# Kernel optimization log

Hardware: AMD Instinct MI355X
Metric: run time of the kernel (lower is better)

Reference implementation:

```python
import jax, jax.numpy as jnp
import numpy as np

SIGMA = 0.1   # sigma_disc (params[3])
ALPHA = 0.05  # alpha_disc (params[2])


def setup_inputs() -> dict:
    key = jax.random.key(0)
    k1, k2, k3 = jax.random.split(key, 3)
    E, S, T = 3, 8192, 100  # num_events, num_samples, num_bin + num_extra_bin
    logits = jax.random.normal(k1, (E, S, T), dtype=jnp.float32)
    event_out = jax.nn.softmax(logits, axis=-1)  # per-event discrete hazard probs, rows sum to 1
    event_times = jax.random.randint(k2, (S, E), 0, 99).astype(jnp.int32)
    labs = jax.random.randint(k3, (S, E), 0, 2).astype(jnp.int32)
    return {"event_out": event_out, "event_times": event_times, "labs": labs,
            "num_bin": 96, "num_extra_bin": 4}


def _c_loss(event_out, event_times, labs, T):
    # cum[e, k, t] = sum(event_out[e, k, :t+1]); risk with cutoff c = 1 - cum[..., c-1]
    cum = jnp.cumsum(event_out, axis=-1)  # (E, S, T)
    E = event_out.shape[0]
    penalty = jnp.float32(0.0)
    for i in range(E):  # small fixed number of events
        c = cum[i]                    # (S, T)
        t = event_times[:, i]         # (S,)
        lab = labs[:, i]              # (S,)
        had = lab == 1
        # ---- forward concordance (had_event branch) ----
        e_f = jnp.minimum(t + 1, T - 1)              # per-reference-sample cutoff, >= 1
        # risk_f[j, k] = 1 - sum(event_out[k, :e_f[j]]) = 1 - cum[k, e_f[j]-1]
        risk_f = 1.0 - c[:, e_f - 1].T               # (S_j, S_k)
        diff_f = risk_f - jnp.diagonal(risk_f)[:, None]  # comp_risk - reference_risk
        # f_compare: t_k > e_j - 1  OR  (t_k == e_j - 1 AND lab_k == 0)
        mask_f = had[:, None] & ((t[None, :] >= e_f[:, None]) |
                                 ((t[None, :] == e_f[:, None] - 1) & (lab[None, :] == 0)))
        penalty = penalty + jnp.sum(jnp.where(mask_f & (diff_f < 0),
                                              jnp.exp(-diff_f / SIGMA), 0.0))
        # ---- backward concordance (back_c branch, active when t_j > 0) ----
        e_b = jnp.minimum(jnp.where(had, t, t + 1), T - 1)
        risk_b = 1.0 - c[:, jnp.maximum(e_b, 1) - 1].T
        diff_b = risk_b - jnp.diagonal(risk_b)[:, None]
        # b_compare: t_k <= e_j - 1 AND lab_k == 1
        mask_b = (t > 0)[:, None] & (t[None, :] <= e_b[:, None] - 1) & (lab[None, :] == 1)
        penalty = penalty + jnp.sum(jnp.where(mask_b & (diff_b > 0),
                                              jnp.exp(diff_b / SIGMA), 0.0))
    return ALPHA * penalty


def reference(event_out, event_times, labs, num_bin, num_extra_bin):
    return _c_loss(event_out, event_times, labs, num_bin + num_extra_bin)
```

## Files before the change

### kernel.cpp

```cpp
#include <hip/hip_runtime.h>

#define E_CONST 3
#define T_CONST 100
#define C10 10.0f
#define ALPHA_C 0.05f
#define SPLIT 4
#define MAXK 8192
#define NGROUP (E_CONST * 2 * T_CONST)

__device__ inline int waveInclScan(int v, int lane) {
    #pragma unroll
    for (int off = 1; off < 64; off <<= 1) {
        int n = __shfl_up(v, off, 64);
        if (lane >= off) v += n;
    }
    return v;
}

__global__ __launch_bounds__(512) void prep_kernel(
    const float* __restrict__ event_out, float* __restrict__ cumT, int S)
{
    __shared__ float tile[64][101];
    const int tid = threadIdx.x;
    const int rowbase = (int)blockIdx.x * 64;
    const float4* __restrict__ src =
        reinterpret_cast<const float4*>(event_out) + (size_t)rowbase * 25;
    for (int idx = tid; idx < 64 * 25; idx += 512) {
        const float4 v = src[idx];
        const int r = idx / 25;
        const int c = idx - r * 25;
        float* d = &tile[r][c * 4];
        d[0] = v.x; d[1] = v.y; d[2] = v.z; d[3] = v.w;
    }
    __syncthreads();
    if (tid < 64) {
        float run = 0.f;
        #pragma unroll 4
        for (int c = 0; c < T_CONST; ++c) { run += tile[tid][c]; tile[tid][c] = run; }
    }
    __syncthreads();
    const int i  = rowbase / S;
    const int s0 = rowbase - i * S;
    float* __restrict__ dst = cumT + (size_t)i * T_CONST * S + s0;
    for (int idx = tid; idx < 64 * T_CONST; idx += 512) {
        const int t = idx >> 6;
        const int r = idx & 63;
        dst[(size_t)t * S + r] = tile[r][t];
    }
}

__global__ __launch_bounds__(256) void thrfill_kernel(
    const float* __restrict__ cumT, const int* __restrict__ et,
    const int* __restrict__ labs, float* __restrict__ thrVals,
    int* __restrict__ gCnt, int S)
{
    __shared__ int wcnt[4];
    const int tid = threadIdx.x;
    const int lane = tid & 63, wid = tid >> 6;
    const int gid = (int)blockIdx.x;
    const int i = gid / 200;
    const int r = gid - i * 200;
    const int dir = r / 100;
    const int tt = r - dir * 100;

    const int colIdx = tt;
    int t1 = 0, t2 = -1;
    bool any = true;
    if (dir == 0) { t1 = tt; }
    else {
        const int cb = tt;
        if (cb >= T_CONST - 1) any = false;
        t1 = cb + 1;
        if (cb > 0) t2 = cb;
    }

    int cnt = 0;
    if (any) {
        const float* __restrict__ col = cumT + ((size_t)i * T_CONST + colIdx) * S;
        float* __restrict__ dst = thrVals + (size_t)gid * MAXK;
        for (int s0 = 0; s0 < S; s0 += 1024) {
            const int sb = s0 + tid * 4;
            const float4 cv = *reinterpret_cast<const float4*>(col + sb);
            float tv[4]; int mask = 0, m = 0;
            #pragma unroll
            for (int j = 0; j < 4; ++j) {
                const int s = sb + j;
                const int ts = et[s * E_CONST + i];
                const int ls = labs[s * E_CONST + i];
                const float c = (j == 0) ? cv.x : (j == 1) ? cv.y
                              : (j == 2) ? cv.z : cv.w;
                tv[j] = __expf(C10 * c);
                const bool p = ((ts == t1) & (ls == 1)) |
                               ((t2 >= 0) & (ts == t2) & (ls == 0));
                if (p) { mask |= (1 << j); ++m; }
            }
            const int incl = waveInclScan(m, lane);
            if (lane == 63) wcnt[wid] = incl;
            __syncthreads();
            int base = cnt + incl - m;
            for (int w = 0; w < wid; ++w) base += wcnt[w];
            #pragma unroll
            for (int j = 0; j < 4; ++j)
                if (mask & (1 << j)) dst[base++] = tv[j];
            cnt += wcnt[0] + wcnt[1] + wcnt[2] + wcnt[3];
            __syncthreads();
        }
    }
    if (tid == 0) gCnt[gid] = cnt;
}

__global__ __launch_bounds__(256) void grouppair_kernel(
    const float* __restrict__ cumT, const float* __restrict__ thrVals,
    const int* __restrict__ gCnt, const int* __restrict__ et,
    const int* __restrict__ labs, float* __restrict__ partials, int S)
{
    __shared__ __align__(16) float elds[2048];
    __shared__ float wsum[4];
    __shared__ int wcnt[4];
    __shared__ int nTot;
    const int tid = threadIdx.x;
    const int lane = tid & 63, wid = tid >> 6;

    int x = (int)blockIdx.x;
    const int sp = x & (SPLIT - 1); x >>= 2;
    const int dir = x & 1;          x >>= 1;
    const int tt = x % T_CONST;
    const int i  = x / T_CONST;

    int colIdx = 0, tref = 0, tgid = 0;
    bool active = true;
    if (dir == 0) { colIdx = tt; tref = tt; tgid = i * 200 + tt; }
    else {
        const int cb = (T_CONST - 2) - tt;
        if (cb < 0) active = false;
        else { colIdx = cb; tref = cb; tgid = i * 200 + 100 + cb; }
    }
    const int K = active ? gCnt[tgid] : 0;
    if (K <= 0) active = false;

    float blocktot = 0.f;
    if (active) {
        const float* __restrict__ col = cumT + ((size_t)i * T_CONST + colIdx) * S;
        const float sgn = (dir == 0) ? C10 : -C10;
        const int chunk = S / SPLIT;
        const int cbeg = sp * chunk;

        float ev[8];
        int mask = 0, m = 0;
        #pragma unroll
        for (int j = 0; j < 8; ++j) {
            const int s = cbeg + tid + j * 256;
            const int ts = et[s * E_CONST + i];
            const int ls = labs[s * E_CONST + i];
            const bool mem = (dir == 0)
                ? ((ts > tref) | ((ts == tref) & (ls == 0)))
                : ((ts <= tref) & (ls == 1));
            ev[j] = __expf(sgn * col[s]);
            if (mem) { mask |= (1 << j); ++m; }
        }
        const int incl = waveInclScan(m, lane);
        if (lane == 63) wcnt[wid] = incl;
        __syncthreads();
        int off = 0;
        for (int w = 0; w < wid; ++w) off += wcnt[w];
        int base = incl - m + off;
        #pragma unroll
        for (int j = 0; j < 8; ++j)
            if (mask & (1 << j)) elds[base++] = ev[j];
        if (tid == 255) {
            nTot = base;
            const int np = (base + 3) & ~3;
            for (int p = base; p < np; ++p) elds[p] = 0.f;
        }
        __syncthreads();

        const int n = nTot;
        if (n > 0) {
            const int qn4 = ((n + 3) & ~3) >> 2;
            const int kq = tid & 31;
            const int ep = tid >> 5;
            const float4* __restrict__ e4 = reinterpret_cast<const float4*>(elds);
            const float* __restrict__ tv = thrVals + (size_t)tgid * MAXK;
            const int nkc = (K + 31) >> 5;

            for (int kc = 0; kc < nkc; ++kc) {
                const int j = (kc << 5) + kq;
                float thr = 1e30f, factor = 0.f;
                if (j < K) {
                    const float tval = tv[j];
                    if (dir == 0) { thr = tval;        factor = 1.0f / tval; }
                    else          { thr = 1.0f / tval; factor = tval; }
                }
                float acc = 0.f;
                for (int q = ep; q < qn4; q += 8) {
                    const float4 v = e4[q];
                    acc += (v.x > thr) ? v.x : 0.f;
                    acc += (v.y > thr) ? v.y : 0.f;
                    acc += (v.z > thr) ? v.z : 0.f;
                    acc += (v.w > thr) ? v.w : 0.f;
                }
                blocktot += acc * factor;
            }
        }
    }

    for (int off = 32; off > 0; off >>= 1) blocktot += __shfl_down(blocktot, off, 64);
    if (lane == 0) wsum[wid] = blocktot;
    __syncthreads();
    if (tid == 0) partials[blockIdx.x] = wsum[0] + wsum[1] + wsum[2] + wsum[3];
}

__global__ __launch_bounds__(1024) void reduce_kernel(
    const float* __restrict__ partials, int n, float* __restrict__ out)
{
    const int tid = threadIdx.x;
    float s0 = 0.f, s1 = 0.f, s2 = 0.f, s3 = 0.f;
    const int n4 = n & ~3;
    for (int idx = tid * 4; idx < n4; idx += 4096) {
        const float4 v = *reinterpret_cast<const float4*>(partials + idx);
        s0 += v.x; s1 += v.y; s2 += v.z; s3 += v.w;
    }
    for (int idx = n4 + tid; idx < n; idx += 1024) s0 += partials[idx];
    float sum = (s0 + s1) + (s2 + s3);
    for (int off = 32; off > 0; off >>= 1) sum += __shfl_down(sum, off, 64);
    __shared__ float wsum[16];
    const int lane = tid & 63, wd = tid >> 6;
    if (lane == 0) wsum[wd] = sum;
    __syncthreads();
    if (tid == 0) {
        float t = 0.f;
        for (int w = 0; w < 16; ++w) t += wsum[w];
        out[0] = ALPHA_C * t;
    }
}

__global__ __launch_bounds__(64) void prep_fb_kernel(
    const float* __restrict__ event_out, const int* __restrict__ et,
    const int* __restrict__ labs, float* __restrict__ cumT,
    int* __restrict__ tlA, int S)
{
    const int gid = blockIdx.x * 64 + threadIdx.x;
    const int i = gid / S;
    const int s = gid - i * S;
    const float4* __restrict__ row =
        reinterpret_cast<const float4*>(event_out + (size_t)gid * T_CONST);
    float* __restrict__ base = cumT + (size_t)i * T_CONST * S + s;
    float run = 0.f;
    #pragma unroll
    for (int c = 0; c < T_CONST / 4; ++c) {
        const float4 v = row[c];
        const float c0 = run + v.x;
        const float c1 = c0 + v.y;
        const float c2 = c1 + v.z;
        const float c3 = c2 + v.w;
        base[(size_t)(4 * c + 0) * S] = c0;
        base[(size_t)(4 * c + 1) * S] = c1;
        base[(size_t)(4 * c + 2) * S] = c2;
        base[(size_t)(4 * c + 3) * S] = c3;
        run = c3;
    }
    const int t   = et[s * E_CONST + i];
    const int lab = labs[s * E_CONST + i];
    tlA[i * S + s] = (t & 0xffff) | (lab << 16);
}

__global__ __launch_bounds__(256) void pair_fb_kernel(
    const float* __restrict__ cumT, const int* __restrict__ tlA,
    float* __restrict__ partials, int S)
{
    const int bx = blockIdx.x;
    const int i = bx / S;
    const int k = bx - i * S;
    const int base = i * S;
    const int tlk = tlA[base + k];
    const int t_k = tlk & 0xffff;
    const int lab_k = tlk >> 16;
    const bool doF = (lab_k == 1);
    const bool doB = (t_k > 0);
    float sum = 0.f;
    if (doF || doB) {
        const int cb = lab_k ? (t_k > 0 ? t_k - 1 : 0) : t_k;
        const float* __restrict__ colF = cumT + ((size_t)i * T_CONST + t_k) * S;
        const float* __restrict__ colB = cumT + ((size_t)i * T_CONST + cb)  * S;
        const float vf_k = colF[k];
        const float vb_k = colB[k];
        const int* __restrict__ tlp = tlA + base;
        for (int s = threadIdx.x; s < S; s += 256) {
            const int tls = tlp[s];
            const int t_s = tls & 0xffff;
            const int lab_s = tls >> 16;
            if (doF) {
                const float vs = colF[s];
                const bool c = (t_s > t_k) | ((t_s == t_k) & (lab_s == 0));
                if (c & (vs > vf_k)) sum += __expf((vs - vf_k) * C10);
            }
            if (doB) {
                const float vs = colB[s];
                const bool c = (t_s <= cb) & (lab_s == 1);
                if (c & (vb_k > vs)) sum += __expf((vb_k - vs) * C10);
            }
        }
    }
    for (int off = 32; off > 0; off >>= 1) sum += __shfl_down(sum, off, 64);
    __shared__ float wsum[4];
    const int lane = threadIdx.x & 63, wd = threadIdx.x >> 6;
    if (lane == 0) wsum[wd] = sum;
    __syncthreads();
    if (threadIdx.x == 0) partials[bx] = wsum[0] + wsum[1] + wsum[2] + wsum[3];
}

extern "C" void kernel_launch(void* const* d_in, const int* in_sizes, int n_in,
                              void* d_out, int out_size, void* d_ws, size_t ws_size,
                              hipStream_t stream)
{
    const float* event_out = (const float*)d_in[0];
    const int*   et        = (const int*)d_in[1];
    const int*   labsp     = (const int*)d_in[2];
    const int S = in_sizes[1] / E_CONST;

    const size_t colElems = (size_t)E_CONST * T_CONST * S;
    const size_t esElems  = (size_t)E_CONST * S;
    const int    gpBlocks = E_CONST * T_CONST * 2 * SPLIT;

    char* p = (char*)d_ws;
    float* cumT     = (float*)p; p += colElems * 4;
    float* thrVals  = (float*)p; p += (size_t)NGROUP * MAXK * 4;
    int*   gCnt     = (int*)p;   p += (size_t)NGROUP * 4;
    float* partials = (float*)p; p += (size_t)gpBlocks * 4;
    const size_t needed = (size_t)(p - (char*)d_ws);
    const size_t fallback_needed = colElems * 4 + esElems * 4 * 2;

    const int prepBlocks = (E_CONST * S) / 64;

    if (ws_size >= needed && (E_CONST * S) % 64 == 0 &&
        (S / SPLIT) == 2048 && (S % 1024) == 0 && S <= MAXK) {
        hipLaunchKernelGGL(prep_kernel, dim3(prepBlocks), dim3(512), 0, stream,
                           event_out, cumT, S);
        hipLaunchKernelGGL(thrfill_kernel, dim3(NGROUP), dim3(256), 0, stream,
                           cumT, et, labsp, thrVals, gCnt, S);
        hipLaunchKernelGGL(grouppair_kernel, dim3(gpBlocks), dim3(256), 0, stream,
                           cumT, thrVals, gCnt, et, labsp, partials, S);
        hipLaunchKernelGGL(reduce_kernel, dim3(1), dim3(1024), 0, stream,
                           partials, gpBlocks, (float*)d_out);
    } else if (ws_size >= fallback_needed) {
        const int nB = E_CONST * S;
        float* cumT2     = (float*)d_ws;
        int*   tlA2      = (int*)(cumT2 + colElems);
        float* partials2 = (float*)(tlA2 + esElems);
        hipLaunchKernelGGL(prep_fb_kernel, dim3(E_CONST * S / 64), dim3(64), 0, stream,
                           event_out, et, labsp, cumT2, tlA2, S);
        hipLaunchKernelGGL(pair_fb_kernel, dim3(nB), dim3(256), 0, stream,
                           cumT2, tlA2, partials2, S);
        hipLaunchKernelGGL(reduce_kernel, dim3(1), dim3(1024), 0, stream,
                           partials2, nB, (float*)d_out);
    }
}
```

Baseline: 116.0 us.

## Fuse cumsum prep and threshold fill into one launch with on-the-fly prefix sums

The separate prep (cumsum/transpose) and threshold-fill kernels are merged into one grid. Blocks past NGROUP do the transposed cumsum with 32-row tiles, and the rest compute threshold values by summing each selected row's prefix straight from event_out. This removes the dependency on cumT inside the fill, which saves one launch and lets both stages overlap. The cost is redundant per-row prefix summation with serial, uncoalesced float4 loads, but only for predicate-selected samples.

```diff
diff --git a/kernel.cpp b/kernel.cpp
--- a/kernel.cpp
+++ b/kernel.cpp
@@ -17,45 +17,44 @@
     return v;
 }
 
-__global__ __launch_bounds__(512) void prep_kernel(
-    const float* __restrict__ event_out, float* __restrict__ cumT, int S)
-{
-    __shared__ float tile[64][101];
-    const int tid = threadIdx.x;
-    const int rowbase = (int)blockIdx.x * 64;
-    const float4* __restrict__ src =
-        reinterpret_cast<const float4*>(event_out) + (size_t)rowbase * 25;
-    for (int idx = tid; idx < 64 * 25; idx += 512) {
-        const float4 v = src[idx];
-        const int r = idx / 25;
-        const int c = idx - r * 25;
-        float* d = &tile[r][c * 4];
-        d[0] = v.x; d[1] = v.y; d[2] = v.z; d[3] = v.w;
-    }
-    __syncthreads();
-    if (tid < 64) {
-        float run = 0.f;
-        #pragma unroll 4
-        for (int c = 0; c < T_CONST; ++c) { run += tile[tid][c]; tile[tid][c] = run; }
-    }
-    __syncthreads();
-    const int i  = rowbase / S;
-    const int s0 = rowbase - i * S;
-    float* __restrict__ dst = cumT + (size_t)i * T_CONST * S + s0;
-    for (int idx = tid; idx < 64 * T_CONST; idx += 512) {
-        const int t = idx >> 6;
-        const int r = idx & 63;
-        dst[(size_t)t * S + r] = tile[r][t];
-    }
-}
-
-__global__ __launch_bounds__(256) void thrfill_kernel(
-    const float* __restrict__ cumT, const int* __restrict__ et,
-    const int* __restrict__ labs, float* __restrict__ thrVals,
-    int* __restrict__ gCnt, int S)
-{
+__global__ __launch_bounds__(256) void combo256_kernel(
+    const float* __restrict__ event_out, const int* __restrict__ et,
+    const int* __restrict__ labs, float* __restrict__ cumT,
+    float* __restrict__ thrVals, int* __restrict__ gCnt, int S)
+{
+    __shared__ float tile[32][101];
     __shared__ int wcnt[4];
     const int tid = threadIdx.x;
+
+    if ((int)blockIdx.x >= NGROUP) {
+        const int rowbase = ((int)blockIdx.x - NGROUP) * 32;
+        const float4* __restrict__ src =
+            reinterpret_cast<const float4*>(event_out) + (size_t)rowbase * 25;
+        for (int idx = tid; idx < 32 * 25; idx += 256) {
+            const float4 v = src[idx];
+            const int r = idx / 25;
+            const int c = idx - r * 25;
+            float* d = &tile[r][c * 4];
+            d[0] = v.x; d[1] = v.y; d[2] = v.z; d[3] = v.w;
+        }
+        __syncthreads();
+        if (tid < 32) {
+            float run = 0.f;
+            #pragma unroll 4
+            for (int c = 0; c < T_CONST; ++c) { run += tile[tid][c]; tile[tid][c] = run; }
+        }
+        __syncthreads();
+        const int i  = rowbase / S;
+        const int s0 = rowbase - i * S;
+        float* __restrict__ dst = cumT + (size_t)i * T_CONST * S + s0;
+        for (int idx = tid; idx < 32 * T_CONST; idx += 256) {
+            const int t = idx >> 5;
+            const int r = idx & 31;
+            dst[(size_t)t * S + r] = tile[r][t];
+        }
+        return;
+    }
+
     const int lane = tid & 63, wid = tid >> 6;
     const int gid = (int)blockIdx.x;
     const int i = gid / 200;
@@ -76,23 +75,37 @@
 
     int cnt = 0;
     if (any) {
-        const float* __restrict__ col = cumT + ((size_t)i * T_CONST + colIdx) * S;
         float* __restrict__ dst = thrVals + (size_t)gid * MAXK;
+        const int nfull = (colIdx + 1) >> 2;
+        const int rem   = (colIdx + 1) & 3;
         for (int s0 = 0; s0 < S; s0 += 1024) {
             const int sb = s0 + tid * 4;
-            const float4 cv = *reinterpret_cast<const float4*>(col + sb);
             float tv[4]; int mask = 0, m = 0;
             #pragma unroll
             for (int j = 0; j < 4; ++j) {
                 const int s = sb + j;
                 const int ts = et[s * E_CONST + i];
                 const int ls = labs[s * E_CONST + i];
-                const float c = (j == 0) ? cv.x : (j == 1) ? cv.y
-                              : (j == 2) ? cv.z : cv.w;
-                tv[j] = __expf(C10 * c);
                 const bool p = ((ts == t1) & (ls == 1)) |
                                ((t2 >= 0) & (ts == t2) & (ls == 0));
-                if (p) { mask |= (1 << j); ++m; }
+                tv[j] = 0.f;
+                if (p) {
+                    const float4* __restrict__ row4 = reinterpret_cast<const float4*>(
+                        event_out + ((size_t)i * S + s) * T_CONST);
+                    float run = 0.f;
+                    for (int c = 0; c < nfull; ++c) {
+                        const float4 v = row4[c];
+                        run += v.x; run += v.y; run += v.z; run += v.w;
+                    }
+                    if (rem) {
+                        const float4 v = row4[nfull];
+                        run += v.x;
+                        if (rem > 1) run += v.y;
+                        if (rem > 2) run += v.z;
+                    }
+                    tv[j] = __expf(C10 * run);
+                    mask |= (1 << j); ++m;
+                }
             }
             const int incl = waveInclScan(m, lane);
             if (lane == 63) wcnt[wid] = incl;
@@ -330,14 +343,12 @@
     const size_t needed = (size_t)(p - (char*)d_ws);
     const size_t fallback_needed = colElems * 4 + esElems * 4 * 2;
 
-    const int prepBlocks = (E_CONST * S) / 64;
-
-    if (ws_size >= needed && (E_CONST * S) % 64 == 0 &&
+    const int prepBlocks = (E_CONST * S) / 32;
+
+    if (ws_size >= needed && (E_CONST * S) % 32 == 0 &&
         (S / SPLIT) == 2048 && (S % 1024) == 0 && S <= MAXK) {
-        hipLaunchKernelGGL(prep_kernel, dim3(prepBlocks), dim3(512), 0, stream,
-                           event_out, cumT, S);
-        hipLaunchKernelGGL(thrfill_kernel, dim3(NGROUP), dim3(256), 0, stream,
-                           cumT, et, labsp, thrVals, gCnt, S);
+        hipLaunchKernelGGL(combo256_kernel, dim3(NGROUP + prepBlocks), dim3(256), 0, stream,
+                           event_out, et, labsp, cumT, thrVals, gCnt, S);
         hipLaunchKernelGGL(grouppair_kernel, dim3(gpBlocks), dim3(256), 0, stream,
                            cumT, thrVals, gCnt, et, labsp, partials, S);
         hipLaunchKernelGGL(reduce_kernel, dim3(1), dim3(1024), 0, stream,
```

Measured after the change: 197.8 us. 70.5% more time.
